# Optimization experiments

Hardware: AMD Instinct MI355X
Metric: run time of the kernel (lower is better)

Reference implementation:

```python
import jax, jax.numpy as jnp
import numpy as np

PHI = 1.6
JITTER = 1e-4
ETA = 1.0
BETA = 0.5
EPS_CHOL = 1e-6
R_NEIGH = 2


def _solve3(L, d):
    # lower-triangular 3x3 forward substitution; L broadcasts against d[..., 3]
    y0 = d[..., 0] / L[..., 0, 0]
    y1 = (d[..., 1] - L[..., 1, 0] * y0) / L[..., 1, 1]
    y2 = (d[..., 2] - L[..., 2, 0] * y0 - L[..., 2, 1] * y1) / L[..., 2, 2]
    return jnp.stack([y0, y1, y2], axis=-1)


def _overlap_score(delta, L):
    # fused_gaussian_overlap_score: Gaussian log-overlap ~ -0.5*(Mahalanobis + logdet)
    y = _solve3(L, delta)
    maha = jnp.sum(y * y, axis=-1)
    logdet = 2.0 * jnp.sum(jnp.log(jnp.diagonal(L, axis1=-2, axis2=-1)), axis=-1)
    return -0.5 * (maha + logdet)


def _head(x, ln_g, ln_b, W1, b1, W2, b2):
    # LayerNorm -> Linear -> SiLU -> Linear(->1), squeeze
    m = jnp.mean(x, axis=-1, keepdims=True)
    v = jnp.var(x, axis=-1, keepdims=True)
    h = (x - m) / jnp.sqrt(v + 1e-5) * ln_g + ln_b
    h = jax.nn.silu(h @ W1 + b1)
    return (h @ W2 + b2)[..., 0]


def setup_inputs() -> dict:
    key = jax.random.key(0)
    ks = jax.random.split(key, 12)
    B, Kp, M, C = 2, 1024, 8, 256
    s_parent = jax.random.normal(ks[0], (B, Kp, C), jnp.float32)
    mu_p = jax.random.normal(ks[1], (B, Kp, 3), jnp.float32) * 10.0
    A = jax.random.normal(ks[2], (B, Kp, 3, 3), jnp.float32) * 0.5
    Sigma_p = jnp.einsum('bkij,bklj->bkil', A, A) + 0.05 * jnp.eye(3, dtype=jnp.float32)
    mask_parent = jnp.ones((B, Kp), jnp.float32)
    xi_noise = jax.random.normal(ks[3], (B, Kp, M, 3), jnp.float32)
    emb = jax.random.normal(ks[4], (M, C), jnp.float32) * 0.02
    lin = lambda k, fi, fo, s=0.02: jax.random.normal(k, (fi, fo), jnp.float32) * s
    return dict(
        s_parent=s_parent, mu_p=mu_p, Sigma_p=Sigma_p, mask_parent=mask_parent,
        xi_noise=xi_noise, emb=emb,
        gate_ln_g=jnp.ones((C,), jnp.float32), gate_ln_b=jnp.zeros((C,), jnp.float32),
        gate_W1=lin(ks[5], C, C), gate_b1=jnp.zeros((C,), jnp.float32),
        gate_W2=lin(ks[6], C, 1), gate_b2=jnp.zeros((1,), jnp.float32),
        prior_ln_g=jnp.ones((C,), jnp.float32), prior_ln_b=jnp.zeros((C,), jnp.float32),
        prior_W1=lin(ks[7], C, C), prior_b1=jnp.zeros((C,), jnp.float32),
        prior_W2=lin(ks[8], C, 1), prior_b2=jnp.zeros((1,), jnp.float32),
        geom_W=lin(ks[9], C, 3, 0.01), geom_b=jnp.zeros((3,), jnp.float32),
        K_target=6144,
    )


def reference(s_parent, mu_p, Sigma_p, mask_parent, xi_noise, emb,
              gate_ln_g, gate_ln_b, gate_W1, gate_b1, gate_W2, gate_b2,
              prior_ln_g, prior_ln_b, prior_W1, prior_b1, prior_W2, prior_b2,
              geom_W, geom_b, K_target):
    B, Kp, C = s_parent.shape
    M = emb.shape[0]
    Kc = Kp * M
    I3 = jnp.eye(3, dtype=s_parent.dtype)

    # --- candidate children from per-parent Cholesky splat ---
    Lp = jnp.linalg.cholesky(Sigma_p + EPS_CHOL * I3)               # [B,Kp,3,3]
    xi = xi_noise + (emb @ geom_W + geom_b)                          # [B,Kp,M,3]
    mu0 = mu_p[:, :, None, :] + jnp.einsum('bkae,bkme->bkma', Lp, xi)
    mu0 = mu0.reshape(B, Kc, 3)

    j0 = jnp.repeat(jnp.arange(Kp), M)                               # [Kc] birth parent
    t_ids = jnp.tile(jnp.arange(M), Kp)                              # [Kc] child slot
    m0 = mask_parent[:, j0]

    # --- gate g ---
    gate_in = s_parent[:, j0, :] + emb[t_ids]                        # [B,Kc,C]
    b = _head(gate_in, gate_ln_g, gate_ln_b, gate_W1, gate_b1, gate_W2, gate_b2)
    a = jax.nn.softplus(_head(s_parent, prior_ln_g, prior_ln_b, prior_W1, prior_b1, prior_W2, prior_b2))
    b = b + BETA * jnp.log(a[:, j0] + 1e-8)
    g = jax.nn.sigmoid(b / max(ETA, 1e-6)) * m0                      # [B,Kc]
    loss_count = jnp.mean((jnp.sum(g, axis=1) - float(K_target)) ** 2)

    # --- top-R neighbor parents by overlap score (indices only, no grad) ---
    mu0_birth = mu_p[:, j0, :]                                       # mu of birth parent
    delta1 = mu0_birth[:, :, None, :] - mu_p[:, None, :, :]          # [B,Kc,Kp,3]
    score1 = _overlap_score(delta1, Lp[:, None])                     # [B,Kc,Kp]
    self_hot = (jnp.arange(Kp)[None, :] == j0[:, None])              # [Kc,Kp]
    score1 = jnp.where(self_hot[None], 1e9, score1)
    _, neigh = jax.lax.top_k(jax.lax.stop_gradient(score1), R_NEIGH) # [B,Kc,R], col0=j0

    bidx = jnp.arange(B)[:, None, None]
    mu_nei = mu_p[bidx, neigh]                                       # [B,Kc,R,3]
    Sig_nei = Sigma_p[bidx, neigh]                                   # [B,Kc,R,3,3]
    L_nei = Lp[bidx, neigh]
    s_nei = s_parent[bidx, neigh]                                    # [B,Kc,R,C]

    # --- soft responsibilities over the R neighbors ---
    score2 = _overlap_score(mu0[:, :, None, :] - mu_nei, L_nei)      # [B,Kc,R]
    w = jax.nn.softmax(score2, axis=-1)

    # --- moment-matching refine (sparse form of B_resp: rows of B are w scattered at neigh) ---
    mu_child = jnp.einsum('bir,bird->bid', w, mu_nei)                # [B,Kc,3]
    intra = jnp.einsum('bir,birmn->bimn', w, Sig_nei) * PHI ** (-2)
    dmu = mu_nei - mu_child[:, :, None, :]
    inter = jnp.einsum('bir,birm,birn->bimn', w, dmu, dmu)
    Sigma_child = intra + inter + JITTER * I3                        # [B,Kc,3,3]

    s_mix = jnp.einsum('bir,birc->bic', w, s_nei)
    s_child0 = g[..., None] * s_mix                                  # [B,Kc,C]
    return s_child0, mu_child, Sigma_child, g, loss_count
```

## Files before the change

kernel.cpp:

```cpp
#include <hip/hip_runtime.h>
#include <math.h>

#define NPAR 2048
#define KP   1024
#define MM   8
#define CC   256
#define KC   8192
#define NCH  16384

#define WS_PAR    0
#define WS_MEANSP 26624
#define WS_SUMSQ  28672
#define WS_DOT8   30720
#define WS_APRIOR 47104
#define WS_EGATE  49152
#define WS_UGATE  51200
#define WS_C0GATE 51456
#define WS_GEO    51712
#define WS_MEANE  51736
#define WS_SUMSQE 51744
#define WS_NEIGH  51752
#define WS_PGATE  53824

#define OUT_S    0
#define OUT_MU   4194304
#define OUT_SIG  4243456
#define OUT_G    4390912
#define OUT_LOSS 4407296

__device__ __forceinline__ float siluf(float x){ return x / (1.f + expf(-x)); }
__device__ __forceinline__ float softplusf(float x){ return x > 20.f ? x : log1pf(expf(x)); }

__global__ __launch_bounds__(256) void kP(const float* __restrict__ sp,
                                          const float* __restrict__ mu_p,
                                          const float* __restrict__ Sig,
                                          const float* __restrict__ emb,
                                          const float* __restrict__ geom_W,
                                          const float* __restrict__ geom_b,
                                          const float* __restrict__ g_ln_g,
                                          const float* __restrict__ g_ln_b,
                                          const float* __restrict__ gW1,
                                          const float* __restrict__ gb1,
                                          const float* __restrict__ p_ln_g,
                                          const float* __restrict__ p_ln_b,
                                          const float* __restrict__ pW1,
                                          const float* __restrict__ pb1,
                                          const float* __restrict__ pW2,
                                          const float* __restrict__ pb2,
                                          float* __restrict__ ws) {
  __shared__ float xs[8][256];
  __shared__ float red[4][8];
  __shared__ float redS[4][8];
  __shared__ float redQ[4][8];
  __shared__ float mv[2][8];
  int blk = blockIdx.x;
  int t = threadIdx.x;

  if (blk < 512) {
    int pid  = blk * 4 + (t >> 6);
    int lane = t & 63;
    const float4 v = *(const float4*)(sp + pid * CC + lane * 4);
    float s  = v.x + v.y + v.z + v.w;
    float ss = v.x*v.x + v.y*v.y + v.z*v.z + v.w*v.w;
    float pd[8];
#pragma unroll
    for (int m = 0; m < 8; m++) {
      float4 e = *(const float4*)(emb + m * CC + lane * 4);
      pd[m] = v.x*e.x + v.y*e.y + v.z*e.z + v.w*e.w;
    }
#pragma unroll
    for (int o = 32; o > 0; o >>= 1) {
      s  += __shfl_xor(s, o);
      ss += __shfl_xor(ss, o);
#pragma unroll
      for (int m = 0; m < 8; m++) pd[m] += __shfl_xor(pd[m], o);
    }
    if (lane == 0) {
      ws[WS_MEANSP + pid] = s * (1.f / 256.f);
      ws[WS_SUMSQ + pid]  = ss;
#pragma unroll
      for (int m = 0; m < 8; m++) ws[WS_DOT8 + pid * 8 + m] = pd[m];
    }
  } else if (blk < 520) {
    int pid = (blk - 512) * 256 + t;
    const float* S = Sig + pid * 9;
    float a00 = S[0] + 1e-6f, a10 = S[3], a11 = S[4] + 1e-6f;
    float a20 = S[6], a21 = S[7], a22 = S[8] + 1e-6f;
    float L00 = sqrtf(a00); float i0 = 1.f / L00;
    float L10 = a10 * i0, L20 = a20 * i0;
    float L11 = sqrtf(a11 - L10 * L10); float i1 = 1.f / L11;
    float L21 = (a21 - L20 * L10) * i1;
    float L22 = sqrtf(a22 - L20 * L20 - L21 * L21); float i2 = 1.f / L22;
    float logdet = 2.f * logf(L00 * L11 * L22);
    float* P = ws + WS_PAR;
    P[0*NPAR+pid]=L00; P[1*NPAR+pid]=L10; P[2*NPAR+pid]=L11;
    P[3*NPAR+pid]=L20; P[4*NPAR+pid]=L21; P[5*NPAR+pid]=L22;
    P[6*NPAR+pid]=i0;  P[7*NPAR+pid]=i1;  P[8*NPAR+pid]=i2;
    P[9*NPAR+pid]=logdet;
    P[10*NPAR+pid]=mu_p[pid*3+0]; P[11*NPAR+pid]=mu_p[pid*3+1]; P[12*NPAR+pid]=mu_p[pid*3+2];
  } else if (blk == 520) {
    if (t < 192) {
      int o = t >> 3, lane8 = t & 7;
      int m = o / 3, d = o % 3;
      float acc = 0.f;
      for (int k = lane8; k < 256; k += 8) acc += emb[m * 256 + k] * geom_W[k * 3 + d];
      acc += __shfl_xor(acc, 1); acc += __shfl_xor(acc, 2); acc += __shfl_xor(acc, 4);
      if (lane8 == 0) ws[WS_GEO + o] = acc + geom_b[d];
    } else {
      int o = (t - 192) >> 3, lane8 = t & 7;
      if (o < 8) {
        float s = 0.f, ss = 0.f;
        for (int k = lane8; k < 256; k += 8) { float e = emb[o * 256 + k]; s += e; ss += e * e; }
        s  += __shfl_xor(s, 1);  s  += __shfl_xor(s, 2);  s  += __shfl_xor(s, 4);
        ss += __shfl_xor(ss, 1); ss += __shfl_xor(ss, 2); ss += __shfl_xor(ss, 4);
        if (lane8 == 0) { ws[WS_MEANE + o] = s * (1.f / 256.f); ws[WS_SUMSQE + o] = ss; }
      }
    }
  } else if (blk < 1033) {
    int wv = (blk - 521) * 4 + (t >> 6);
    int lane = t & 63;
    int b = wv >> 10;
    int j = wv & (KP - 1);
    float qx = mu_p[wv*3+0], qy = mu_p[wv*3+1], qz = mu_p[wv*3+2];
    float best = -3.4e38f; int bidx = 1 << 30;
    for (int it = 0; it < 16; it++) {
      int k = it * 64 + lane;
      int idx = b * KP + k;
      const float* S = Sig + idx * 9;
      float a00 = S[0] + 1e-6f, a10 = S[3], a11 = S[4] + 1e-6f;
      float a20 = S[6], a21 = S[7], a22 = S[8] + 1e-6f;
      float L00 = sqrtf(a00); float i0 = 1.f / L00;
      float L10 = a10 * i0, L20 = a20 * i0;
      float L11 = sqrtf(a11 - L10 * L10); float i1 = 1.f / L11;
      float L21 = (a21 - L20 * L10) * i1;
      float L22 = sqrtf(a22 - L20 * L20 - L21 * L21); float i2 = 1.f / L22;
      float ld = 2.f * logf(L00 * L11 * L22);
      float dx = qx - mu_p[idx*3+0], dy = qy - mu_p[idx*3+1], dz = qz - mu_p[idx*3+2];
      float y0 = dx * i0;
      float y1 = (dy - L10 * y0) * i1;
      float y2 = (dz - L20 * y0 - L21 * y1) * i2;
      float sc = -0.5f * (y0*y0 + y1*y1 + y2*y2 + ld);
      if (k == j) sc = -3.4e38f;
      if (sc > best || (sc == best && k < bidx)) { best = sc; bidx = k; }
    }
#pragma unroll
    for (int o = 32; o > 0; o >>= 1) {
      float ob = __shfl_xor(best, o);
      int   oi = __shfl_xor(bidx, o);
      if (ob > best || (ob == best && oi < bidx)) { best = ob; bidx = oi; }
    }
    if (lane == 0) ((int*)ws)[WS_NEIGH + wv] = bidx;
  } else {
    int cblk = blk - 1033;
    bool prior = (cblk >= 256 && cblk < 512);
    const float* W1 = prior ? pW1 : gW1;

    if (cblk < 256) {
      int base = cblk * 8;
      float g = g_ln_g[t];
#pragma unroll
      for (int r = 0; r < 8; r++) xs[r][t] = sp[(base + r) * 256 + t] * g;
    } else if (cblk < 512) {
      int base = (cblk - 256) * 8;
      float vr[8], s1[8], s2[8];
#pragma unroll
      for (int r = 0; r < 8; r++) {
        vr[r] = sp[(base + r) * 256 + t];
        s1[r] = vr[r];
        s2[r] = vr[r] * vr[r];
      }
#pragma unroll
      for (int o = 32; o > 0; o >>= 1) {
#pragma unroll
        for (int r = 0; r < 8; r++) { s1[r] += __shfl_xor(s1[r], o); s2[r] += __shfl_xor(s2[r], o); }
      }
      int wave = t >> 6;
      if ((t & 63) == 0) {
#pragma unroll
        for (int r = 0; r < 8; r++) { redS[wave][r] = s1[r]; redQ[wave][r] = s2[r]; }
      }
      __syncthreads();
      if (t < 8) {
        float sum = redS[0][t] + redS[1][t] + redS[2][t] + redS[3][t];
        float sq  = redQ[0][t] + redQ[1][t] + redQ[2][t] + redQ[3][t];
        float mean = sum * (1.f / 256.f);
        float var  = sq * (1.f / 256.f) - mean * mean;
        mv[0][t] = mean;
        mv[1][t] = rsqrtf(var + 1e-5f);
      }
      __syncthreads();
      float pg = p_ln_g[t], pbv = p_ln_b[t];
#pragma unroll
      for (int r = 0; r < 8; r++)
        xs[r][t] = (vr[r] - mv[0][r]) * mv[1][r] * pg + pbv;
    } else if (cblk == 512) {
      float g = g_ln_g[t];
#pragma unroll
      for (int r = 0; r < 8; r++) xs[r][t] = emb[r * 256 + t] * g;
    } else {
      xs[0][t] = g_ln_g[t];
      xs[1][t] = g_ln_b[t];
#pragma unroll
      for (int r = 2; r < 8; r++) xs[r][t] = 0.f;
    }
    __syncthreads();

    float acc[8] = {0,0,0,0,0,0,0,0};
    for (int k = 0; k < 256; k++) {
      float w = W1[k * 256 + t];
#pragma unroll
      for (int r = 0; r < 8; r++) acc[r] += xs[r][k] * w;
    }

    if (cblk < 256) {
      int base = cblk * 8;
#pragma unroll
      for (int r = 0; r < 8; r++) ws[WS_PGATE + (base + r) * 256 + t] = acc[r];
    } else if (cblk < 512) {
      int base = (cblk - 256) * 8;
      float b1 = pb1[t], w2 = pW2[t];
      float tv[8];
#pragma unroll
      for (int r = 0; r < 8; r++) {
        float h = acc[r] + b1;
        tv[r] = siluf(h) * w2;
      }
#pragma unroll
      for (int o = 32; o > 0; o >>= 1) {
#pragma unroll
        for (int r = 0; r < 8; r++) tv[r] += __shfl_xor(tv[r], o);
      }
      int wave = t >> 6;
      if ((t & 63) == 0) {
#pragma unroll
        for (int r = 0; r < 8; r++) red[wave][r] = tv[r];
      }
      __syncthreads();
      if (t < 8) {
        float sum = red[0][t] + red[1][t] + red[2][t] + red[3][t] + pb2[0];
        ws[WS_APRIOR + base + t] = softplusf(sum);
      }
    } else if (cblk == 512) {
#pragma unroll
      for (int r = 0; r < 8; r++) ws[WS_EGATE + r * 256 + t] = acc[r];
    } else {
      ws[WS_UGATE + t]  = acc[0];
      ws[WS_C0GATE + t] = acc[1] + gb1[t];
    }
  }
}

__global__ __launch_bounds__(256) void kD(const float* __restrict__ sp,
                                          const float* __restrict__ Sig,
                                          const float* __restrict__ mask,
                                          const float* __restrict__ xi_noise,
                                          const float* __restrict__ gW2,
                                          const float* __restrict__ gb2,
                                          const float* __restrict__ ws,
                                          float* __restrict__ out) {
  int wv   = blockIdx.x * 4 + (threadIdx.x >> 6);
  int lane = threadIdx.x & 63;
  int b = wv >> 13;
  int i = wv & (KC - 1);
  int j = i >> 3;
  int m = i & 7;
  int prow = b * KP + j;

  float mean_x = ws[WS_MEANSP + prow] + ws[WS_MEANE + m];
  float Ex2 = ws[WS_SUMSQ + prow] + 2.f * ws[WS_DOT8 + prow * 8 + m] + ws[WS_SUMSQE + m];
  float var = Ex2 * (1.f / 256.f) - mean_x * mean_x;
  float rstd = rsqrtf(var + 1e-5f);

  int c4 = lane * 4;
  float Pv[4], Ev[4], Uv[4], C0v[4], W2v[4];
  *(float4*)Pv  = *(const float4*)(ws + WS_PGATE + prow * 256 + c4);
  *(float4*)Ev  = *(const float4*)(ws + WS_EGATE + m * 256 + c4);
  *(float4*)Uv  = *(const float4*)(ws + WS_UGATE + c4);
  *(float4*)C0v = *(const float4*)(ws + WS_C0GATE + c4);
  *(float4*)W2v = *(const float4*)(gW2 + c4);
  float partial = 0.f;
#pragma unroll
  for (int q = 0; q < 4; q++) {
    float pre = (Pv[q] + Ev[q] - mean_x * Uv[q]) * rstd + C0v[q];
    partial += siluf(pre) * W2v[q];
  }
#pragma unroll
  for (int o = 32; o > 0; o >>= 1) partial += __shfl_xor(partial, o);
  float aP = ws[WS_APRIOR + prow];
  float bval = partial + gb2[0] + 0.5f * logf(aP + 1e-8f);
  float g = (1.f / (1.f + expf(-bval))) * mask[prow];

  const float* PP = ws + WS_PAR;
  float L00 = PP[0*NPAR+prow], L10 = PP[1*NPAR+prow], L11 = PP[2*NPAR+prow];
  float L20 = PP[3*NPAR+prow], L21 = PP[4*NPAR+prow], L22 = PP[5*NPAR+prow];
  float mx = PP[10*NPAR+prow], my = PP[11*NPAR+prow], mz = PP[12*NPAR+prow];
  int xbase = (prow * 8 + m) * 3;
  float x0 = xi_noise[xbase + 0] + ws[WS_GEO + m * 3 + 0];
  float x1 = xi_noise[xbase + 1] + ws[WS_GEO + m * 3 + 1];
  float x2 = xi_noise[xbase + 2] + ws[WS_GEO + m * 3 + 2];
  float m0x = mx + L00 * x0;
  float m0y = my + L10 * x0 + L11 * x1;
  float m0z = mz + L20 * x0 + L21 * x1 + L22 * x2;

  int n1 = ((const int*)ws)[WS_NEIGH + prow];
  int nrow[2]; nrow[0] = prow; nrow[1] = b * KP + n1;
  float sc[2], nx[2], ny[2], nz[2];
#pragma unroll
  for (int r = 0; r < 2; r++) {
    int q = nrow[r];
    float i0 = PP[6*NPAR+q], i1 = PP[7*NPAR+q], i2 = PP[8*NPAR+q], ld = PP[9*NPAR+q];
    float l10 = PP[1*NPAR+q], l20 = PP[3*NPAR+q], l21 = PP[4*NPAR+q];
    nx[r] = PP[10*NPAR+q]; ny[r] = PP[11*NPAR+q]; nz[r] = PP[12*NPAR+q];
    float dx = m0x - nx[r], dy = m0y - ny[r], dz = m0z - nz[r];
    float y0 = dx * i0;
    float y1 = (dy - l10 * y0) * i1;
    float y2 = (dz - l20 * y0 - l21 * y1) * i2;
    sc[r] = -0.5f * (y0*y0 + y1*y1 + y2*y2 + ld);
  }
  float mxs = fmaxf(sc[0], sc[1]);
  float e0 = expf(sc[0] - mxs), e1 = expf(sc[1] - mxs);
  float inv = 1.f / (e0 + e1);
  float w0 = e0 * inv, w1 = e1 * inv;

  float mcx = w0 * nx[0] + w1 * nx[1];
  float mcy = w0 * ny[0] + w1 * ny[1];
  float mcz = w0 * nz[0] + w1 * nz[1];

  float d0x = nx[0] - mcx, d0y = ny[0] - mcy, d0z = nz[0] - mcz;
  float d1x = nx[1] - mcx, d1y = ny[1] - mcy, d1z = nz[1] - mcz;
  const float* S0 = Sig + nrow[0] * 9;
  const float* S1 = Sig + nrow[1] * 9;
  const float PHIm2 = 0.390625f;
  float Sout[9];
  float dd0[3] = {d0x, d0y, d0z};
  float dd1[3] = {d1x, d1y, d1z};
#pragma unroll
  for (int a = 0; a < 3; a++)
#pragma unroll
    for (int e = 0; e < 3; e++) {
      float v = (w0 * S0[a*3+e] + w1 * S1[a*3+e]) * PHIm2
              + w0 * dd0[a] * dd0[e] + w1 * dd1[a] * dd1[e];
      if (a == e) v += 1e-4f;
      Sout[a*3+e] = v;
    }

  if (lane == 0) {
    float* om = out + OUT_MU + wv * 3;
    om[0] = mcx; om[1] = mcy; om[2] = mcz;
    out[OUT_G + wv] = g;
    float* os = out + OUT_SIG + wv * 9;
#pragma unroll
    for (int q = 0; q < 9; q++) os[q] = Sout[q];
  }

  float s0v[4], s1v[4], ov[4];
  *(float4*)s0v = *(const float4*)(sp + nrow[0] * 256 + c4);
  *(float4*)s1v = *(const float4*)(sp + nrow[1] * 256 + c4);
  float gw0 = g * w0, gw1 = g * w1;
#pragma unroll
  for (int q = 0; q < 4; q++) ov[q] = gw0 * s0v[q] + gw1 * s1v[q];
  *(float4*)(out + OUT_S + wv * 256 + c4) = *(float4*)ov;
}

__global__ __launch_bounds__(256) void kF(const float* __restrict__ out_in,
                                          const int* __restrict__ Kt,
                                          float* __restrict__ out) {
  __shared__ float red[4][2];
  int t = threadIdx.x;
  const float* gp = out_in + OUT_G;
  float s0 = 0.f, s1 = 0.f;
  for (int it = 0; it < 32; it++) {
    s0 += gp[it * 256 + t];
    s1 += gp[KC + it * 256 + t];
  }
#pragma unroll
  for (int o = 32; o > 0; o >>= 1) {
    s0 += __shfl_xor(s0, o);
    s1 += __shfl_xor(s1, o);
  }
  int wave = t >> 6;
  if ((t & 63) == 0) { red[wave][0] = s0; red[wave][1] = s1; }
  __syncthreads();
  if (t == 0) {
    float S0 = red[0][0] + red[1][0] + red[2][0] + red[3][0];
    float S1 = red[0][1] + red[1][1] + red[2][1] + red[3][1];
    float K = (float)Kt[0];
    float l0 = S0 - K, l1 = S1 - K;
    out[OUT_LOSS] = 0.5f * (l0 * l0 + l1 * l1);
  }
}

extern "C" void kernel_launch(void* const* d_in, const int* in_sizes, int n_in,
                              void* d_out, int out_size, void* d_ws, size_t ws_size,
                              hipStream_t stream) {
  const float* s_parent   = (const float*)d_in[0];
  const float* mu_p       = (const float*)d_in[1];
  const float* Sigma_p    = (const float*)d_in[2];
  const float* mask_par   = (const float*)d_in[3];
  const float* xi_noise   = (const float*)d_in[4];
  const float* emb        = (const float*)d_in[5];
  const float* gate_ln_g  = (const float*)d_in[6];
  const float* gate_ln_b  = (const float*)d_in[7];
  const float* gate_W1    = (const float*)d_in[8];
  const float* gate_b1    = (const float*)d_in[9];
  const float* gate_W2    = (const float*)d_in[10];
  const float* gate_b2    = (const float*)d_in[11];
  const float* prior_ln_g = (const float*)d_in[12];
  const float* prior_ln_b = (const float*)d_in[13];
  const float* prior_W1   = (const float*)d_in[14];
  const float* prior_b1   = (const float*)d_in[15];
  const float* prior_W2   = (const float*)d_in[16];
  const float* prior_b2   = (const float*)d_in[17];
  const float* geom_W     = (const float*)d_in[18];
  const float* geom_b     = (const float*)d_in[19];
  const int*   K_target   = (const int*)d_in[20];

  float* ws  = (float*)d_ws;
  float* out = (float*)d_out;

  kP<<<1547, 256, 0, stream>>>(s_parent, mu_p, Sigma_p, emb, geom_W, geom_b,
                               gate_ln_g, gate_ln_b, gate_W1, gate_b1,
                               prior_ln_g, prior_ln_b, prior_W1, prior_b1,
                               prior_W2, prior_b2, ws);
  kD<<<NCH / 4, 256, 0, stream>>>(s_parent, Sigma_p, mask_par, xi_noise,
                                  gate_W2, gate_b2, ws, out);
  kF<<<1, 256, 0, stream>>>(out, K_target, out);
}
```

Before: 147.1 us.

## Split prep kernel so neighbor search reuses precomputed packed Cholesky factors

Splits the prep kernel in two. The first computes per-parent Cholesky factors, inverses, logdet and means into packed float4 workspace records. The second runs the nearest-neighbor search from those records, so it no longer recomputes the sqrt, log and divide for every pair. The gate and prior GEMM loop is also unrolled by four using float4 shared-memory reads, and the main kernel reads the packed records with vector loads. In exchange this adds a kernel launch and a serial dependency between the two prep kernels.

```diff
diff --git a/kernel.cpp b/kernel.cpp
--- a/kernel.cpp
+++ b/kernel.cpp
@@ -8,7 +8,10 @@
 #define KC   8192
 #define NCH  16384
 
-#define WS_PAR    0
+#define WS_PKL    0
+#define WS_PKI    8192
+#define WS_PKM    16384
+#define WS_L22    24576
 #define WS_MEANSP 26624
 #define WS_SUMSQ  28672
 #define WS_DOT8   30720
@@ -31,31 +34,15 @@
 __device__ __forceinline__ float siluf(float x){ return x / (1.f + expf(-x)); }
 __device__ __forceinline__ float softplusf(float x){ return x > 20.f ? x : log1pf(expf(x)); }
 
-__global__ __launch_bounds__(256) void kP(const float* __restrict__ sp,
-                                          const float* __restrict__ mu_p,
-                                          const float* __restrict__ Sig,
-                                          const float* __restrict__ emb,
-                                          const float* __restrict__ geom_W,
-                                          const float* __restrict__ geom_b,
-                                          const float* __restrict__ g_ln_g,
-                                          const float* __restrict__ g_ln_b,
-                                          const float* __restrict__ gW1,
-                                          const float* __restrict__ gb1,
-                                          const float* __restrict__ p_ln_g,
-                                          const float* __restrict__ p_ln_b,
-                                          const float* __restrict__ pW1,
-                                          const float* __restrict__ pb1,
-                                          const float* __restrict__ pW2,
-                                          const float* __restrict__ pb2,
-                                          float* __restrict__ ws) {
-  __shared__ float xs[8][256];
-  __shared__ float red[4][8];
-  __shared__ float redS[4][8];
-  __shared__ float redQ[4][8];
-  __shared__ float mv[2][8];
+__global__ __launch_bounds__(256) void kP1(const float* __restrict__ sp,
+                                           const float* __restrict__ mu_p,
+                                           const float* __restrict__ Sig,
+                                           const float* __restrict__ emb,
+                                           const float* __restrict__ geom_W,
+                                           const float* __restrict__ geom_b,
+                                           float* __restrict__ ws) {
   int blk = blockIdx.x;
   int t = threadIdx.x;
-
   if (blk < 512) {
     int pid  = blk * 4 + (t >> 6);
     int lane = t & 63;
@@ -92,13 +79,14 @@
     float L21 = (a21 - L20 * L10) * i1;
     float L22 = sqrtf(a22 - L20 * L20 - L21 * L21); float i2 = 1.f / L22;
     float logdet = 2.f * logf(L00 * L11 * L22);
-    float* P = ws + WS_PAR;
-    P[0*NPAR+pid]=L00; P[1*NPAR+pid]=L10; P[2*NPAR+pid]=L11;
-    P[3*NPAR+pid]=L20; P[4*NPAR+pid]=L21; P[5*NPAR+pid]=L22;
-    P[6*NPAR+pid]=i0;  P[7*NPAR+pid]=i1;  P[8*NPAR+pid]=i2;
-    P[9*NPAR+pid]=logdet;
-    P[10*NPAR+pid]=mu_p[pid*3+0]; P[11*NPAR+pid]=mu_p[pid*3+1]; P[12*NPAR+pid]=mu_p[pid*3+2];
-  } else if (blk == 520) {
+    float4 pkl = {L10, L20, L21, logdet};
+    float4 pki = {i0, i1, i2, L00};
+    float4 pkm = {mu_p[pid*3+0], mu_p[pid*3+1], mu_p[pid*3+2], L11};
+    *(float4*)(ws + WS_PKL + pid * 4) = pkl;
+    *(float4*)(ws + WS_PKI + pid * 4) = pki;
+    *(float4*)(ws + WS_PKM + pid * 4) = pkm;
+    ws[WS_L22 + pid] = L22;
+  } else {
     if (t < 192) {
       int o = t >> 3, lane8 = t & 7;
       int m = o / 3, d = o % 3;
@@ -116,30 +104,49 @@
         if (lane8 == 0) { ws[WS_MEANE + o] = s * (1.f / 256.f); ws[WS_SUMSQE + o] = ss; }
       }
     }
-  } else if (blk < 1033) {
-    int wv = (blk - 521) * 4 + (t >> 6);
+  }
+}
+
+__global__ __launch_bounds__(256) void kP2(const float* __restrict__ sp,
+                                           const float* __restrict__ emb,
+                                           const float* __restrict__ g_ln_g,
+                                           const float* __restrict__ g_ln_b,
+                                           const float* __restrict__ gW1,
+                                           const float* __restrict__ gb1,
+                                           const float* __restrict__ p_ln_g,
+                                           const float* __restrict__ p_ln_b,
+                                           const float* __restrict__ pW1,
+                                           const float* __restrict__ pb1,
+                                           const float* __restrict__ pW2,
+                                           const float* __restrict__ pb2,
+                                           float* __restrict__ ws) {
+  __shared__ float xs[8][256];
+  __shared__ float red[4][8];
+  __shared__ float redS[4][8];
+  __shared__ float redQ[4][8];
+  __shared__ float mv[2][8];
+  int blk = blockIdx.x;
+  int t = threadIdx.x;
+
+  if (blk < 512) {
+    int wv = blk * 4 + (t >> 6);
     int lane = t & 63;
     int b = wv >> 10;
     int j = wv & (KP - 1);
-    float qx = mu_p[wv*3+0], qy = mu_p[wv*3+1], qz = mu_p[wv*3+2];
+    const float4 qm = *(const float4*)(ws + WS_PKM + wv * 4);
+    float qx = qm.x, qy = qm.y, qz = qm.z;
     float best = -3.4e38f; int bidx = 1 << 30;
     for (int it = 0; it < 16; it++) {
       int k = it * 64 + lane;
       int idx = b * KP + k;
-      const float* S = Sig + idx * 9;
-      float a00 = S[0] + 1e-6f, a10 = S[3], a11 = S[4] + 1e-6f;
-      float a20 = S[6], a21 = S[7], a22 = S[8] + 1e-6f;
-      float L00 = sqrtf(a00); float i0 = 1.f / L00;
-      float L10 = a10 * i0, L20 = a20 * i0;
-      float L11 = sqrtf(a11 - L10 * L10); float i1 = 1.f / L11;
-      float L21 = (a21 - L20 * L10) * i1;
-      float L22 = sqrtf(a22 - L20 * L20 - L21 * L21); float i2 = 1.f / L22;
-      float ld = 2.f * logf(L00 * L11 * L22);
-      float dx = qx - mu_p[idx*3+0], dy = qy - mu_p[idx*3+1], dz = qz - mu_p[idx*3+2];
-      float y0 = dx * i0;
-      float y1 = (dy - L10 * y0) * i1;
-      float y2 = (dz - L20 * y0 - L21 * y1) * i2;
-      float sc = -0.5f * (y0*y0 + y1*y1 + y2*y2 + ld);
+      float4 pl = *(const float4*)(ws + WS_PKL + idx * 4);
+      float4 pi = *(const float4*)(ws + WS_PKI + idx * 4);
+      float4 pm = *(const float4*)(ws + WS_PKM + idx * 4);
+      float dx = qx - pm.x, dy = qy - pm.y, dz = qz - pm.z;
+      float y0 = dx * pi.x;
+      float y1 = (dy - pl.x * y0) * pi.y;
+      float y2 = (dz - pl.y * y0 - pl.z * y1) * pi.z;
+      float sc = -0.5f * (y0*y0 + y1*y1 + y2*y2 + pl.w);
       if (k == j) sc = -3.4e38f;
       if (sc > best || (sc == best && k < bidx)) { best = sc; bidx = k; }
     }
@@ -151,7 +158,7 @@
     }
     if (lane == 0) ((int*)ws)[WS_NEIGH + wv] = bidx;
   } else {
-    int cblk = blk - 1033;
+    int cblk = blk - 512;
     bool prior = (cblk >= 256 && cblk < 512);
     const float* W1 = prior ? pW1 : gW1;
 
@@ -206,10 +213,16 @@
     __syncthreads();
 
     float acc[8] = {0,0,0,0,0,0,0,0};
-    for (int k = 0; k < 256; k++) {
-      float w = W1[k * 256 + t];
-#pragma unroll
-      for (int r = 0; r < 8; r++) acc[r] += xs[r][k] * w;
+    for (int k4 = 0; k4 < 256; k4 += 4) {
+      float w0 = W1[(k4+0) * 256 + t];
+      float w1 = W1[(k4+1) * 256 + t];
+      float w2 = W1[(k4+2) * 256 + t];
+      float w3 = W1[(k4+3) * 256 + t];
+#pragma unroll
+      for (int r = 0; r < 8; r++) {
+        float4 x4 = *(const float4*)&xs[r][k4];
+        acc[r] += x4.x * w0 + x4.y * w1 + x4.z * w2 + x4.w * w3;
+      }
     }
 
     if (cblk < 256) {
@@ -290,32 +303,41 @@
   float bval = partial + gb2[0] + 0.5f * logf(aP + 1e-8f);
   float g = (1.f / (1.f + expf(-bval))) * mask[prow];
 
-  const float* PP = ws + WS_PAR;
-  float L00 = PP[0*NPAR+prow], L10 = PP[1*NPAR+prow], L11 = PP[2*NPAR+prow];
-  float L20 = PP[3*NPAR+prow], L21 = PP[4*NPAR+prow], L22 = PP[5*NPAR+prow];
-  float mx = PP[10*NPAR+prow], my = PP[11*NPAR+prow], mz = PP[12*NPAR+prow];
+  const float4 plP = *(const float4*)(ws + WS_PKL + prow * 4);
+  const float4 piP = *(const float4*)(ws + WS_PKI + prow * 4);
+  const float4 pmP = *(const float4*)(ws + WS_PKM + prow * 4);
+  float L22 = ws[WS_L22 + prow];
+
   int xbase = (prow * 8 + m) * 3;
   float x0 = xi_noise[xbase + 0] + ws[WS_GEO + m * 3 + 0];
   float x1 = xi_noise[xbase + 1] + ws[WS_GEO + m * 3 + 1];
   float x2 = xi_noise[xbase + 2] + ws[WS_GEO + m * 3 + 2];
-  float m0x = mx + L00 * x0;
-  float m0y = my + L10 * x0 + L11 * x1;
-  float m0z = mz + L20 * x0 + L21 * x1 + L22 * x2;
+  float m0x = pmP.x + piP.w * x0;
+  float m0y = pmP.y + plP.x * x0 + pmP.w * x1;
+  float m0z = pmP.z + plP.y * x0 + plP.z * x1 + L22 * x2;
 
   int n1 = ((const int*)ws)[WS_NEIGH + prow];
-  int nrow[2]; nrow[0] = prow; nrow[1] = b * KP + n1;
+  int nrow1 = b * KP + n1;
+  const float4 plN = *(const float4*)(ws + WS_PKL + nrow1 * 4);
+  const float4 piN = *(const float4*)(ws + WS_PKI + nrow1 * 4);
+  const float4 pmN = *(const float4*)(ws + WS_PKM + nrow1 * 4);
+
   float sc[2], nx[2], ny[2], nz[2];
-#pragma unroll
-  for (int r = 0; r < 2; r++) {
-    int q = nrow[r];
-    float i0 = PP[6*NPAR+q], i1 = PP[7*NPAR+q], i2 = PP[8*NPAR+q], ld = PP[9*NPAR+q];
-    float l10 = PP[1*NPAR+q], l20 = PP[3*NPAR+q], l21 = PP[4*NPAR+q];
-    nx[r] = PP[10*NPAR+q]; ny[r] = PP[11*NPAR+q]; nz[r] = PP[12*NPAR+q];
-    float dx = m0x - nx[r], dy = m0y - ny[r], dz = m0z - nz[r];
-    float y0 = dx * i0;
-    float y1 = (dy - l10 * y0) * i1;
-    float y2 = (dz - l20 * y0 - l21 * y1) * i2;
-    sc[r] = -0.5f * (y0*y0 + y1*y1 + y2*y2 + ld);
+  {
+    float dx = m0x - pmP.x, dy = m0y - pmP.y, dz = m0z - pmP.z;
+    float y0 = dx * piP.x;
+    float y1 = (dy - plP.x * y0) * piP.y;
+    float y2 = (dz - plP.y * y0 - plP.z * y1) * piP.z;
+    sc[0] = -0.5f * (y0*y0 + y1*y1 + y2*y2 + plP.w);
+    nx[0] = pmP.x; ny[0] = pmP.y; nz[0] = pmP.z;
+  }
+  {
+    float dx = m0x - pmN.x, dy = m0y - pmN.y, dz = m0z - pmN.z;
+    float y0 = dx * piN.x;
+    float y1 = (dy - plN.x * y0) * piN.y;
+    float y2 = (dz - plN.y * y0 - plN.z * y1) * piN.z;
+    sc[1] = -0.5f * (y0*y0 + y1*y1 + y2*y2 + plN.w);
+    nx[1] = pmN.x; ny[1] = pmN.y; nz[1] = pmN.z;
   }
   float mxs = fmaxf(sc[0], sc[1]);
   float e0 = expf(sc[0] - mxs), e1 = expf(sc[1] - mxs);
@@ -328,8 +350,8 @@
 
   float d0x = nx[0] - mcx, d0y = ny[0] - mcy, d0z = nz[0] - mcz;
   float d1x = nx[1] - mcx, d1y = ny[1] - mcy, d1z = nz[1] - mcz;
-  const float* S0 = Sig + nrow[0] * 9;
-  const float* S1 = Sig + nrow[1] * 9;
+  const float* S0 = Sig + prow * 9;
+  const float* S1 = Sig + nrow1 * 9;
   const float PHIm2 = 0.390625f;
   float Sout[9];
   float dd0[3] = {d0x, d0y, d0z};
@@ -354,8 +376,8 @@
   }
 
   float s0v[4], s1v[4], ov[4];
-  *(float4*)s0v = *(const float4*)(sp + nrow[0] * 256 + c4);
-  *(float4*)s1v = *(const float4*)(sp + nrow[1] * 256 + c4);
+  *(float4*)s0v = *(const float4*)(sp + prow * 256 + c4);
+  *(float4*)s1v = *(const float4*)(sp + nrow1 * 256 + c4);
   float gw0 = g * w0, gw1 = g * w1;
 #pragma unroll
   for (int q = 0; q < 4; q++) ov[q] = gw0 * s0v[q] + gw1 * s1v[q];
@@ -418,10 +440,10 @@
   float* ws  = (float*)d_ws;
   float* out = (float*)d_out;
 
-  kP<<<1547, 256, 0, stream>>>(s_parent, mu_p, Sigma_p, emb, geom_W, geom_b,
-                               gate_ln_g, gate_ln_b, gate_W1, gate_b1,
-                               prior_ln_g, prior_ln_b, prior_W1, prior_b1,
-                               prior_W2, prior_b2, ws);
+  kP1<<<521, 256, 0, stream>>>(s_parent, mu_p, Sigma_p, emb, geom_W, geom_b, ws);
+  kP2<<<1026, 256, 0, stream>>>(s_parent, emb, gate_ln_g, gate_ln_b, gate_W1, gate_b1,
+                                prior_ln_g, prior_ln_b, prior_W1, prior_b1,
+                                prior_W2, prior_b2, ws);
   kD<<<NCH / 4, 256, 0, stream>>>(s_parent, Sigma_p, mask_par, xi_noise,
                                   gate_W2, gate_b2, ws, out);
   kF<<<1, 256, 0, stream>>>(out, K_target, out);
```

New measurement: 146.2 us, median of 2. Within noise of the previous version (-0.6%).
